# Kernel tuning notes

Hardware: AMD Instinct MI355X
Metric: run time of the kernel (lower is better)

The kernel has to match this reference:

```python
import math
import jax
import jax.numpy as jnp
import numpy as np

DECAY_RATE = 0.99
LOG_CLAMP_MIN = -10.0


def setup_inputs() -> dict:
    key = jax.random.key(0)
    k0, k1, k2, k3, k4, k5 = jax.random.split(key, 6)
    B, S, D, N = 32, 4096, 256, 64
    return {
        "query": jax.random.normal(k0, (B, S, D), dtype=jnp.float32),
        "memory": jax.random.normal(k1, (1, N, D), dtype=jnp.float32),
        "importance": jax.random.uniform(k2, (1, N), dtype=jnp.float32),
        "age": jax.random.uniform(k3, (1, N), dtype=jnp.float32) * 10.0,
        # torch.nn.Linear weights are [out_features, in_features]; applied as x @ W.T
        "W_q": jax.random.normal(k4, (D, D), dtype=jnp.float32) / jnp.sqrt(D).astype(jnp.float32),
        "W_k": jax.random.normal(k5, (D, D), dtype=jnp.float32) / jnp.sqrt(D).astype(jnp.float32),
        "top_k": 8,
    }


def reference(query, memory, importance, age, W_q, W_k, top_k):
    # MemoryBank.read(): top-k masked attention over a small memory bank
    # query: [B, S, D]; memory: [1, N, D]; importance/age: [1, N]
    D = query.shape[-1]
    N = memory.shape[1]
    mem = memory[0]          # [N, D] (buffer is batch-broadcast in torch via expand)

    q = query @ W_q.T                      # [B, S, D]
    k = mem @ W_k.T                        # [N, D]
    scores = jnp.einsum("bsd,nd->bsn", q, k) / jnp.sqrt(jnp.asarray(D, query.dtype))

    # importance-decay bias, log-clamped at -10
    eff_imp = importance[0] * (DECAY_RATE ** age[0])           # [N]
    scores = scores + jnp.maximum(jnp.log(eff_imp), LOG_CLAMP_MIN)[None, None, :]

    if top_k < N:
        _, topk_idx = jax.lax.top_k(scores, top_k)             # [B, S, k]
        # scatter 1.0 at top-k indices (N is small, one-hot sum is cheap)
        mask = jax.nn.one_hot(topk_idx, N, dtype=scores.dtype).sum(axis=-2)  # [B, S, N]
        scores = jnp.where(mask > 0, scores, -jnp.inf)

    attn_weights = jax.nn.softmax(scores, axis=-1)             # [B, S, N]
    retrieved = jnp.einsum("bsn,nd->bsd", attn_weights, mem)   # [B, S, D]
    return retrieved, attn_weights
```

## Files before the change

### kernel.cpp

```cpp
#include <hip/hip_runtime.h>
#include <hip/hip_bf16.h>

#define DD 256
#define NM 64

typedef unsigned long long u64;
typedef float v2f __attribute__((ext_vector_type(2)));

struct v2x2 { v2f lo, hi; };
static __device__ __forceinline__ v2x2 splitf4(float4 f) {
    union { float4 a; v2x2 b; } u; u.a = f; return u.b;
}

#define PK_FMA_SPLATLO(acc, q2, c2) \
    asm("v_pk_fma_f32 %0, %1, %2, %0 op_sel:[0,0,0] op_sel_hi:[0,1,1]" \
        : "+v"(acc) : "v"(q2), "v"(c2))
#define PK_FMA_SPLATHI(acc, q2, c2) \
    asm("v_pk_fma_f32 %0, %1, %2, %0 op_sel:[1,0,0] op_sel_hi:[1,1,1]" \
        : "+v"(acc) : "v"(q2), "v"(c2))

__global__ __launch_bounds__(256) void prep_tr(
    const float* __restrict__ Wq, const float* __restrict__ Wk,
    float* __restrict__ wqt, float* __restrict__ wkt)
{
    const int o = blockIdx.x;
    const int d = threadIdx.x;
    if (blockIdx.y == 0) wqt[d * DD + o] = Wq[o * DD + d];
    else                 wkt[d * DD + o] = Wk[o * DD + d];
}

__global__ __launch_bounds__(256) void prep_kT(
    const float* __restrict__ mem, const float* __restrict__ wkt,
    const float* __restrict__ imp, const float* __restrict__ age,
    float* __restrict__ kT4, float* __restrict__ bias)
{
    const int n = blockIdx.x;
    const int o = threadIdx.x;
    const float* mrow = mem + n * DD;
    float acc = 0.f;
    for (int d = 0; d < DD; ++d)
        acc = fmaf(mrow[d], wkt[d * DD + o], acc);
    kT4[(o >> 2) * (NM * 4) + n * 4 + (o & 3)] = acc;

    if (o == 0) {
        double eff = (double)imp[n] * pow(0.99, (double)age[n]);
        float b = (float)log(eff);
        if (!(b >= -10.0f)) b = -10.0f;
        bias[n] = b;
    }
}

__global__ __launch_bounds__(256, 2) void qgemm5(
    const float* __restrict__ query,
    const float4* __restrict__ wqt4,
    float* __restrict__ qout,
    int M)
{
    __shared__ float wq_lds[2][8 * 256];
    __shared__ float qc_lds[2][64 * 8];

    const int t = threadIdx.x;
    const int l = t & 63;
    const int w = __builtin_amdgcn_readfirstlane((int)(t >> 6));
    const int row0 = blockIdx.x * 64;

    const int sr = t >> 2;
    const int sd = (t & 3) * 2;
    int srow = row0 + sr; if (srow > M - 1) srow = M - 1;
    const float* qsrc = query + (size_t)srow * DD + sd;

    {
        const float2 qv = *reinterpret_cast<const float2*>(qsrc);
        *reinterpret_cast<float2*>(&qc_lds[0][sr * 8 + sd]) = qv;
        const float4 s0 = wqt4[t];
        const float4 s1 = wqt4[256 + t];
        reinterpret_cast<float4*>(wq_lds[0])[t]       = s0;
        reinterpret_cast<float4*>(wq_lds[0])[256 + t] = s1;
    }
    __syncthreads();

    v2f a01[16], a23[16];
#pragma unroll
    for (int rr = 0; rr < 16; ++rr) { a01[rr] = (v2f)(0.f); a23[rr] = (v2f)(0.f); }

    for (int c = 0; c < 32; ++c) {
        const int cn = (c + 1) & 31;
        const float2 nq = *reinterpret_cast<const float2*>(qsrc + cn * 8);
        const float4 n0 = wqt4[cn * 512 + t];
        const float4 n1 = wqt4[cn * 512 + 256 + t];

        {
            const float4* wb = reinterpret_cast<const float4*>(wq_lds[c & 1]);
            float4 cw[8];
#pragma unroll
            for (int i = 0; i < 8; ++i) cw[i] = wb[i * 64 + l];
            const v2x2 c0 = splitf4(cw[0]), c1 = splitf4(cw[1]);
            const v2x2 c2 = splitf4(cw[2]), c3 = splitf4(cw[3]);
            const v2x2 c4 = splitf4(cw[4]), c5 = splitf4(cw[5]);
            const v2x2 c6 = splitf4(cw[6]), c7 = splitf4(cw[7]);
            const float* qcb = &qc_lds[c & 1][(w * 16) * 8];
#pragma unroll
            for (int rr = 0; rr < 16; ++rr) {
                const float4 qqA = *reinterpret_cast<const float4*>(
                    qcb + rr * 8);
                const float4 qqB = *reinterpret_cast<const float4*>(
                    qcb + rr * 8 + 4);
                const v2x2 qA = splitf4(qqA);
                const v2x2 qB = splitf4(qqB);
                PK_FMA_SPLATLO(a01[rr], qA.lo, c0.lo);
                PK_FMA_SPLATLO(a23[rr], qA.lo, c0.hi);
                PK_FMA_SPLATHI(a01[rr], qA.lo, c1.lo);
                PK_FMA_SPLATHI(a23[rr], qA.lo, c1.hi);
                PK_FMA_SPLATLO(a01[rr], qA.hi, c2.lo);
                PK_FMA_SPLATLO(a23[rr], qA.hi, c2.hi);
                PK_FMA_SPLATHI(a01[rr], qA.hi, c3.lo);
                PK_FMA_SPLATHI(a23[rr], qA.hi, c3.hi);
                PK_FMA_SPLATLO(a01[rr], qB.lo, c4.lo);
                PK_FMA_SPLATLO(a23[rr], qB.lo, c4.hi);
                PK_FMA_SPLATHI(a01[rr], qB.lo, c5.lo);
                PK_FMA_SPLATHI(a23[rr], qB.lo, c5.hi);
                PK_FMA_SPLATLO(a01[rr], qB.hi, c6.lo);
                PK_FMA_SPLATLO(a23[rr], qB.hi, c6.hi);
                PK_FMA_SPLATHI(a01[rr], qB.hi, c7.lo);
                PK_FMA_SPLATHI(a23[rr], qB.hi, c7.hi);
            }
        }
        {
            *reinterpret_cast<float2*>(&qc_lds[(c + 1) & 1][sr * 8 + sd]) = nq;
            float4* dst = reinterpret_cast<float4*>(wq_lds[(c + 1) & 1]);
            dst[t]       = n0;
            dst[256 + t] = n1;
        }
        __syncthreads();
    }

#pragma unroll
    for (int rr = 0; rr < 16; ++rr) {
        const int grow = row0 + w * 16 + rr;
        if (grow < M) {
            float4 v; v.x = a01[rr].x; v.y = a01[rr].y; v.z = a23[rr].x; v.w = a23[rr].y;
            *reinterpret_cast<float4*>(&qout[(size_t)grow * DD + 4 * l]) = v;
        }
    }
}

__global__ __launch_bounds__(512, 2) void scores_b(
    const float* __restrict__ qin,
    const float4* __restrict__ kT44,
    const float* __restrict__ bias,
    float* __restrict__ sout,
    int M)
{
    __shared__ float q_lds[64 * DD];
    const int t = threadIdx.x;
    const int l = t & 63;
    const int w = __builtin_amdgcn_readfirstlane((int)(t >> 6));
    const int row0 = blockIdx.x * 64;

    {
        const float4* q4g = reinterpret_cast<const float4*>(qin);
#pragma unroll
        for (int i = 0; i < 8; ++i) {
            const int idx = i * 512 + t;
            const int r = idx >> 6, c4 = idx & 63;
            int gr = row0 + r; if (gr > M - 1) gr = M - 1;
            *reinterpret_cast<float4*>(&q_lds[r * DD + ((c4 ^ r) & 63) * 4]) =
                q4g[(size_t)gr * 64 + c4];
        }
    }
    __syncthreads();

    const int nb = w * 8;
    float sc[8];
#pragma unroll
    for (int j = 0; j < 8; ++j) sc[j] = 0.f;

    for (int og = 0; og < DD / 4; ++og) {
        const float4 q4 = *reinterpret_cast<const float4*>(
            &q_lds[l * DD + (((og ^ l) & 63) << 2)]);
        const float4* ktp = kT44 + og * NM + nb;
#pragma unroll
        for (int j = 0; j < 8; ++j) {
            const float4 kt = ktp[j];
            float v = sc[j];
            v = fmaf(q4.x, kt.x, v);
            v = fmaf(q4.y, kt.y, v);
            v = fmaf(q4.z, kt.z, v);
            v = fmaf(q4.w, kt.w, v);
            sc[j] = v;
        }
    }
    __syncthreads();

    float* s_tmp = q_lds;
#pragma unroll
    for (int j = 0; j < 8; ++j)
        s_tmp[l * NM + ((nb + j + l) & 63)] = sc[j] * 0.0625f + bias[nb + j];
    __syncthreads();

#pragma unroll
    for (int i = 0; i < 8; ++i) {
        const int idx = i * 512 + t;
        const int r = idx >> 6, n = idx & 63;
        const int grow = row0 + r;
        if (grow < M) sout[(size_t)grow * NM + n] = s_tmp[r * NM + ((n + r) & 63)];
    }
}

#define FR 128
__global__ __launch_bounds__(256, 2) void fin3(
    const float* __restrict__ mem,
    const int* __restrict__ topk_p,
    float* __restrict__ out_ret,
    float* __restrict__ out_attn,
    int M)
{
    __shared__ float s_lds[FR * NM];
    __shared__ int   sel_i[FR * 16];
    __shared__ float sel_w[FR * 16];

    const int t = threadIdx.x;
    const int l = t & 63;
    const int w = __builtin_amdgcn_readfirstlane((int)(t >> 6));
    const int row0 = blockIdx.x * FR;
    const int k = *topk_p;

    {
#pragma unroll
        for (int i = 0; i < (FR * NM / 4) / 256; ++i) {
            const int idx = i * 256 + t;
            const int r = idx >> 4, c4 = idx & 15;
            int gr = row0 + r; if (gr > M - 1) gr = M - 1;
            const float4 v = *reinterpret_cast<const float4*>(
                &out_attn[(size_t)gr * NM + c4 * 4]);
            s_lds[r * NM + ((c4 * 4 + 0 + r) & 63)] = v.x;
            s_lds[r * NM + ((c4 * 4 + 1 + r) & 63)] = v.y;
            s_lds[r * NM + ((c4 * 4 + 2 + r) & 63)] = v.z;
            s_lds[r * NM + ((c4 * 4 + 3 + r) & 63)] = v.w;
        }
    }
    __syncthreads();

    if (t < FR) {
        const int r = t;
        float sv[NM];
#pragma unroll
        for (int n = 0; n < NM; ++n) sv[n] = s_lds[r * NM + ((n + r) & 63)];

        if (k < NM) {
            const int kk = k < 16 ? k : 16;
            u64 taken = 0ull;
            float mmax = 0.f, Z = 0.f;
            for (int i = 0; i < kk; ++i) {
                float m = -1.0e30f;
                int idx = 0;
#pragma unroll
                for (int n = 0; n < NM; ++n) {
                    const bool avail  = ((taken >> n) & 1ull) == 0ull;
                    const bool better = avail && (sv[n] > m);
                    m   = better ? sv[n] : m;
                    idx = better ? n : idx;
                }
                taken |= (1ull << idx);
                if (i == 0) mmax = m;
                const float wv = expf(m - mmax);
                Z += wv;
                sel_i[r * 16 + i] = idx;
                sel_w[r * 16 + i] = wv;
            }
#pragma unroll
            for (int n = 0; n < NM; ++n) s_lds[r * NM + ((n + r) & 63)] = 0.f;
            for (int i = 0; i < kk; ++i) {
                const float wz = sel_w[r * 16 + i] / Z;
                sel_w[r * 16 + i] = wz;
                s_lds[r * NM + ((sel_i[r * 16 + i] + r) & 63)] = wz;
            }
        } else {
            float m = -1.0e30f;
#pragma unroll
            for (int n = 0; n < NM; ++n) m = sv[n] > m ? sv[n] : m;
            float Z = 0.f;
#pragma unroll
            for (int n = 0; n < NM; ++n) Z += expf(sv[n] - m);
#pragma unroll
            for (int n = 0; n < NM; ++n) s_lds[r * NM + ((n + r) & 63)] = expf(sv[n] - m) / Z;
        }
    }
    __syncthreads();

#pragma unroll
    for (int i = 0; i < (FR * NM) / 256; ++i) {
        const int idx = i * 256 + t;
        const int r = idx >> 6, n = idx & 63;
        const int grow = row0 + r;
        if (grow < M) out_attn[(size_t)grow * NM + n] = s_lds[r * NM + ((n + r) & 63)];
    }

    {
        const float4* mem4 = reinterpret_cast<const float4*>(mem);
        const int kk = k < 16 ? k : 16;
#pragma unroll 1
        for (int rr = 0; rr < FR / 4; ++rr) {
            const int r    = w * (FR / 4) + rr;
            const int grow = row0 + r;
            if (grow >= M) continue;
            float4 acc; acc.x = 0.f; acc.y = 0.f; acc.z = 0.f; acc.w = 0.f;
            if (k < NM) {
                for (int i = 0; i < kk; ++i) {
                    const int   mi = sel_i[r * 16 + i];
                    const float wz = sel_w[r * 16 + i];
                    const float4 mv = mem4[mi * 64 + l];
                    acc.x = fmaf(wz, mv.x, acc.x);
                    acc.y = fmaf(wz, mv.y, acc.y);
                    acc.z = fmaf(wz, mv.z, acc.z);
                    acc.w = fmaf(wz, mv.w, acc.w);
                }
            } else {
                for (int n = 0; n < NM; ++n) {
                    const float wz = s_lds[r * NM + ((n + r) & 63)];
                    const float4 mv = mem4[n * 64 + l];
                    acc.x = fmaf(wz, mv.x, acc.x);
                    acc.y = fmaf(wz, mv.y, acc.y);
                    acc.z = fmaf(wz, mv.z, acc.z);
                    acc.w = fmaf(wz, mv.w, acc.w);
                }
            }
            *reinterpret_cast<float4*>(&out_ret[(size_t)grow * DD + 4 * l]) = acc;
        }
    }
}

extern "C" void kernel_launch(void* const* d_in, const int* in_sizes, int n_in,
                              void* d_out, int out_size, void* d_ws, size_t ws_size,
                              hipStream_t stream) {
    const float* query      = (const float*)d_in[0];
    const float* memory     = (const float*)d_in[1];
    const float* importance = (const float*)d_in[2];
    const float* age        = (const float*)d_in[3];
    const float* Wq         = (const float*)d_in[4];
    const float* Wk         = (const float*)d_in[5];
    const int*   topk       = (const int*)d_in[6];

    const int M = in_sizes[0] / DD;

    float* kT4  = (float*)d_ws;
    float* bias = kT4 + (size_t)DD * NM;
    float* wqt  = bias + 64;
    float* wkt  = wqt + (size_t)DD * DD;

    hipLaunchKernelGGL(prep_tr, dim3(DD, 2), dim3(DD), 0, stream,
                       Wq, Wk, wqt, wkt);
    hipLaunchKernelGGL(prep_kT, dim3(NM), dim3(DD), 0, stream,
                       memory, wkt, importance, age, kT4, bias);

    float* out_ret  = (float*)d_out;
    float* out_attn = out_ret + (size_t)M * DD;

    hipLaunchKernelGGL(qgemm5, dim3((M + 63) / 64), dim3(256), 0, stream,
                       query, (const float4*)wqt, out_ret, M);
    hipLaunchKernelGGL(scores_b, dim3((M + 63) / 64), dim3(512), 0, stream,
                       out_ret, (const float4*)kT4, bias, out_attn, M);
    hipLaunchKernelGGL(fin3, dim3((M + FR - 1) / FR), dim3(256), 0, stream,
                       memory, topk, out_ret, out_attn, M);
}
```

Before: 385.1 us.

## Fuse scores kernel with top-k softmax and retrieval kernel

```diff
diff --git a/kernel.cpp b/kernel.cpp
--- a/kernel.cpp
+++ b/kernel.cpp
@@ -101,10 +101,8 @@
             const float* qcb = &qc_lds[c & 1][(w * 16) * 8];
 #pragma unroll
             for (int rr = 0; rr < 16; ++rr) {
-                const float4 qqA = *reinterpret_cast<const float4*>(
-                    qcb + rr * 8);
-                const float4 qqB = *reinterpret_cast<const float4*>(
-                    qcb + rr * 8 + 4);
+                const float4 qqA = *reinterpret_cast<const float4*>(qcb + rr * 8);
+                const float4 qqB = *reinterpret_cast<const float4*>(qcb + rr * 8 + 4);
                 const v2x2 qA = splitf4(qqA);
                 const v2x2 qB = splitf4(qqB);
                 PK_FMA_SPLATLO(a01[rr], qA.lo, c0.lo);
@@ -144,18 +142,26 @@
     }
 }
 
-__global__ __launch_bounds__(512, 2) void scores_b(
+__global__ __launch_bounds__(512, 2) void sfin2(
     const float* __restrict__ qin,
+    const float* __restrict__ mem,
     const float4* __restrict__ kT44,
     const float* __restrict__ bias,
-    float* __restrict__ sout,
+    const int* __restrict__ topk_p,
+    float* __restrict__ out_ret,
+    float* __restrict__ out_attn,
     int M)
 {
     __shared__ float q_lds[64 * DD];
+    float* s_tmp = q_lds;
+    int*   sel_i = (int*)(q_lds + 64 * NM);
+    float* sel_w = q_lds + 64 * NM + 64 * 16;
+
     const int t = threadIdx.x;
     const int l = t & 63;
     const int w = __builtin_amdgcn_readfirstlane((int)(t >> 6));
     const int row0 = blockIdx.x * 64;
+    const int k = *topk_p;
 
     {
         const float4* q4g = reinterpret_cast<const float4*>(qin);
@@ -192,60 +198,16 @@
     }
     __syncthreads();
 
-    float* s_tmp = q_lds;
 #pragma unroll
     for (int j = 0; j < 8; ++j)
         s_tmp[l * NM + ((nb + j + l) & 63)] = sc[j] * 0.0625f + bias[nb + j];
     __syncthreads();
 
-#pragma unroll
-    for (int i = 0; i < 8; ++i) {
-        const int idx = i * 512 + t;
-        const int r = idx >> 6, n = idx & 63;
-        const int grow = row0 + r;
-        if (grow < M) sout[(size_t)grow * NM + n] = s_tmp[r * NM + ((n + r) & 63)];
-    }
-}
-
-#define FR 128
-__global__ __launch_bounds__(256, 2) void fin3(
-    const float* __restrict__ mem,
-    const int* __restrict__ topk_p,
-    float* __restrict__ out_ret,
-    float* __restrict__ out_attn,
-    int M)
-{
-    __shared__ float s_lds[FR * NM];
-    __shared__ int   sel_i[FR * 16];
-    __shared__ float sel_w[FR * 16];
-
-    const int t = threadIdx.x;
-    const int l = t & 63;
-    const int w = __builtin_amdgcn_readfirstlane((int)(t >> 6));
-    const int row0 = blockIdx.x * FR;
-    const int k = *topk_p;
-
-    {
-#pragma unroll
-        for (int i = 0; i < (FR * NM / 4) / 256; ++i) {
-            const int idx = i * 256 + t;
-            const int r = idx >> 4, c4 = idx & 15;
-            int gr = row0 + r; if (gr > M - 1) gr = M - 1;
-            const float4 v = *reinterpret_cast<const float4*>(
-                &out_attn[(size_t)gr * NM + c4 * 4]);
-            s_lds[r * NM + ((c4 * 4 + 0 + r) & 63)] = v.x;
-            s_lds[r * NM + ((c4 * 4 + 1 + r) & 63)] = v.y;
-            s_lds[r * NM + ((c4 * 4 + 2 + r) & 63)] = v.z;
-            s_lds[r * NM + ((c4 * 4 + 3 + r) & 63)] = v.w;
-        }
-    }
-    __syncthreads();
-
-    if (t < FR) {
+    if (t < 64) {
         const int r = t;
         float sv[NM];
 #pragma unroll
-        for (int n = 0; n < NM; ++n) sv[n] = s_lds[r * NM + ((n + r) & 63)];
+        for (int n = 0; n < NM; ++n) sv[n] = s_tmp[r * NM + ((n + r) & 63)];
 
         if (k < NM) {
             const int kk = k < 16 ? k : 16;
@@ -269,11 +231,11 @@
                 sel_w[r * 16 + i] = wv;
             }
 #pragma unroll
-            for (int n = 0; n < NM; ++n) s_lds[r * NM + ((n + r) & 63)] = 0.f;
+            for (int n = 0; n < NM; ++n) s_tmp[r * NM + ((n + r) & 63)] = 0.f;
             for (int i = 0; i < kk; ++i) {
                 const float wz = sel_w[r * 16 + i] / Z;
                 sel_w[r * 16 + i] = wz;
-                s_lds[r * NM + ((sel_i[r * 16 + i] + r) & 63)] = wz;
+                s_tmp[r * NM + ((sel_i[r * 16 + i] + r) & 63)] = wz;
             }
         } else {
             float m = -1.0e30f;
@@ -283,25 +245,25 @@
 #pragma unroll
             for (int n = 0; n < NM; ++n) Z += expf(sv[n] - m);
 #pragma unroll
-            for (int n = 0; n < NM; ++n) s_lds[r * NM + ((n + r) & 63)] = expf(sv[n] - m) / Z;
-        }
-    }
-    __syncthreads();
-
-#pragma unroll
-    for (int i = 0; i < (FR * NM) / 256; ++i) {
-        const int idx = i * 256 + t;
+            for (int n = 0; n < NM; ++n) s_tmp[r * NM + ((n + r) & 63)] = expf(sv[n] - m) / Z;
+        }
+    }
+    __syncthreads();
+
+#pragma unroll
+    for (int i = 0; i < 8; ++i) {
+        const int idx = i * 512 + t;
         const int r = idx >> 6, n = idx & 63;
         const int grow = row0 + r;
-        if (grow < M) out_attn[(size_t)grow * NM + n] = s_lds[r * NM + ((n + r) & 63)];
+        if (grow < M) out_attn[(size_t)grow * NM + n] = s_tmp[r * NM + ((n + r) & 63)];
     }
 
     {
         const float4* mem4 = reinterpret_cast<const float4*>(mem);
         const int kk = k < 16 ? k : 16;
 #pragma unroll 1
-        for (int rr = 0; rr < FR / 4; ++rr) {
-            const int r    = w * (FR / 4) + rr;
+        for (int rr = 0; rr < 8; ++rr) {
+            const int r    = w * 8 + rr;
             const int grow = row0 + r;
             if (grow >= M) continue;
             float4 acc; acc.x = 0.f; acc.y = 0.f; acc.z = 0.f; acc.w = 0.f;
@@ -317,7 +279,7 @@
                 }
             } else {
                 for (int n = 0; n < NM; ++n) {
-                    const float wz = s_lds[r * NM + ((n + r) & 63)];
+                    const float wz = s_tmp[r * NM + ((n + r) & 63)];
                     const float4 mv = mem4[n * 64 + l];
                     acc.x = fmaf(wz, mv.x, acc.x);
                     acc.y = fmaf(wz, mv.y, acc.y);
@@ -358,8 +320,7 @@
 
     hipLaunchKernelGGL(qgemm5, dim3((M + 63) / 64), dim3(256), 0, stream,
                        query, (const float4*)wqt, out_ret, M);
-    hipLaunchKernelGGL(scores_b, dim3((M + 63) / 64), dim3(512), 0, stream,
-                       out_ret, (const float4*)kT4, bias, out_attn, M);
-    hipLaunchKernelGGL(fin3, dim3((M + FR - 1) / FR), dim3(256), 0, stream,
-                       memory, topk, out_ret, out_attn, M);
-}
+    hipLaunchKernelGGL(sfin2, dim3((M + 63) / 64), dim3(512), 0, stream,
+                       out_ret, memory, (const float4*)kT4, bias, topk,
+                       out_ret, out_attn, M);
+}
```

Result: slower. 490.0 us (+27.2%).
